# Optimization experiments

Measured on AMD Instinct MI355X. Metric: run time of the kernel, lower is better.

## Reference

```python
import jax, jax.numpy as jnp
import numpy as np

E, C, F, K = 8, 768, 3072, 2  # NUM_EXPERTS, EMBED_DIM, FFN_DIM, TOP_K


def setup_inputs() -> dict:
    key = jax.random.key(0)
    k0, k1, k2, k3 = jax.random.split(key, 4)
    B, T = 8, 2048
    return {
        "x": jax.random.normal(k0, (B, T, C), jnp.float32),
        "router_w": jax.random.normal(k1, (E, C), jnp.float32) * 0.02,
        "w1": jax.random.normal(k2, (E, C, F), jnp.float32) * 0.02,
        "b1": jnp.zeros((E, F), jnp.float32),
        "w2": jax.random.normal(k3, (E, F, C), jnp.float32) * 0.02,
        "b2": jnp.zeros((E, C), jnp.float32),
    }


def reference(x, router_w, w1, b1, w2, b2):
    # Dropout is inference-mode identity (eval). GELU is torch's exact (erf) variant.
    B, T, Cc = x.shape
    flat = x.reshape(-1, Cc)                                   # [N, C]
    logits = flat @ router_w.T                                 # [N, E]
    probs = jax.nn.softmax(logits.astype(jnp.float32), axis=-1)
    top_w, top_i = jax.lax.top_k(probs, K)                     # [N, K]
    top_w = (top_w / top_w.sum(-1, keepdims=True)).astype(x.dtype)
    out = jnp.zeros_like(flat)
    for e in range(E):
        # per-token combine weight for expert e (0 if token not routed to e)
        w_e = jnp.sum(top_w * (top_i == e), axis=-1)[:, None]  # [N, 1]
        h = jax.nn.gelu(flat @ w1[e] + b1[e], approximate=False)  # [N, F]
        out = out + w_e * (h @ w2[e] + b2[e])
    return out.reshape(B, T, Cc)
```

## Files before the change

### kernel.cpp

```cpp
#include <hip/hip_runtime.h>
#include <hip/hip_bf16.h>

#define NTOK 16384
#define CDIM 768
#define FDIM 3072
#define NEXP 8
#define NSLOT 32768
#define HBLK 128
#define MAXT256 135

typedef __attribute__((ext_vector_type(8))) short bf16x8;
typedef __attribute__((ext_vector_type(4))) float f32x4;
typedef __attribute__((ext_vector_type(8))) unsigned short u16x8;

__device__ __forceinline__ unsigned short f2bf(float f) {
  unsigned int u = __float_as_uint(f);
  u += 0x7FFFu + ((u >> 16) & 1u);
  return (unsigned short)(u >> 16);
}
__device__ __forceinline__ float bf2f(unsigned short h) {
  return __uint_as_float((unsigned int)h << 16);
}

__device__ __forceinline__ float fast_gelu(float x) {
  float x2 = x * x;
  float z = x * __builtin_fmaf(0.070565402f, x2, 1.5975981f);
  float s = __builtin_amdgcn_rcpf(1.0f + __expf(-z));
  return x * s;
}

__device__ __forceinline__ void async16(const void* g, void* l) {
  __builtin_amdgcn_global_load_lds(
      (const __attribute__((address_space(1))) unsigned int*)g,
      (__attribute__((address_space(3))) unsigned int*)l, 16, 0, 0);
}

#define BARRIER() asm volatile("s_barrier" ::: "memory")
#define VMC(n)    asm volatile("s_waitcnt vmcnt(" #n ")" ::: "memory")

__global__ __launch_bounds__(256)
void k_transpose(const float* __restrict__ src, unsigned short* __restrict__ dst,
                 int R, int Cc)
{
  __shared__ float tle[32][33];
  int e = blockIdx.z;
  int c0 = blockIdx.x * 32, r0 = blockIdx.y * 32;
  int tx = threadIdx.x & 31, ty = threadIdx.x >> 5;
  const float* s = src + (size_t)e * R * Cc;
  unsigned short* d = dst + (size_t)e * R * Cc;
#pragma unroll
  for (int i = 0; i < 4; ++i)
    tle[ty + i * 8][tx] = s[(size_t)(r0 + ty + i * 8) * Cc + c0 + tx];
  __syncthreads();
#pragma unroll
  for (int i = 0; i < 4; ++i)
    d[(size_t)(c0 + ty + i * 8) * R + r0 + tx] = f2bf(tle[tx][ty + i * 8]);
}

__global__ __launch_bounds__(256)
void k_router(const float* __restrict__ x, const float* __restrict__ rw,
              int* __restrict__ tk_e, float* __restrict__ tk_w)
{
  __shared__ float srw[NEXP * CDIM];
  int tid = threadIdx.x;
#pragma unroll
  for (int i = 0; i < (NEXP * CDIM / 4) / 256; ++i)
    ((float4*)srw)[tid + i * 256] = ((const float4*)rw)[tid + i * 256];
  __syncthreads();
  int lane = tid & 63, wid = tid >> 6;
  int t = blockIdx.x * 4 + wid;
  float a[NEXP];
#pragma unroll
  for (int e = 0; e < NEXP; ++e) a[e] = 0.f;
  const float* xr = x + (size_t)t * CDIM;
#pragma unroll
  for (int c = 0; c < CDIM / 64; ++c) {
    float xv = xr[c * 64 + lane];
#pragma unroll
    for (int e = 0; e < NEXP; ++e) a[e] += xv * srw[e * CDIM + c * 64 + lane];
  }
#pragma unroll
  for (int e = 0; e < NEXP; ++e) {
#pragma unroll
    for (int off = 32; off; off >>= 1) a[e] += __shfl_xor(a[e], off);
  }
  if (lane == 0) {
    int i0 = 0; float l0 = a[0];
#pragma unroll
    for (int e = 1; e < NEXP; ++e) if (a[e] > l0) { l0 = a[e]; i0 = e; }
    int i1 = -1; float l1 = -1e30f;
#pragma unroll
    for (int e = 0; e < NEXP; ++e) if (e != i0 && a[e] > l1) { l1 = a[e]; i1 = e; }
    float w0 = 1.f / (1.f + expf(l1 - l0));
    tk_e[2 * t] = i0;     tk_e[2 * t + 1] = i1;
    tk_w[2 * t] = w0;     tk_w[2 * t + 1] = 1.f - w0;
  }
}

__global__ __launch_bounds__(256)
void k_hist(const int* __restrict__ tk_e, int* __restrict__ blockhist)
{
  __shared__ int h[NEXP];
  int tid = threadIdx.x;
  if (tid < NEXP) h[tid] = 0;
  __syncthreads();
  int e = tk_e[blockIdx.x * 256 + tid];
  atomicAdd(&h[e], 1);
  __syncthreads();
  if (tid < NEXP) blockhist[blockIdx.x * NEXP + tid] = h[tid];
}

__global__ __launch_bounds__(512)
void k_scan2(const int* __restrict__ blockhist, int* __restrict__ counts,
             int* __restrict__ offsets, int* __restrict__ tp,
             int* __restrict__ blockbase)
{
  __shared__ int ltot[NEXP];
  __shared__ int loff[NEXP + 1];
  int tid = threadIdx.x;
  int lane = tid & 63, e = tid >> 6;
  int o0 = blockhist[lane * NEXP + e];
  int o1 = blockhist[(64 + lane) * NEXP + e];
  int h0 = o0, h1 = o1;
#pragma unroll
  for (int d = 1; d < 64; d <<= 1) { int v = __shfl_up(h0, d); if (lane >= d) h0 += v; }
  int s0 = __shfl(h0, 63);
#pragma unroll
  for (int d = 1; d < 64; d <<= 1) { int v = __shfl_up(h1, d); if (lane >= d) h1 += v; }
  h1 += s0;
  if (lane == 63) ltot[e] = h1;
  __syncthreads();
  if (tid == 0) {
    loff[0] = 0;
    int tpv = 0; tp[0] = 0;
    for (int k = 0; k < NEXP; ++k) {
      loff[k + 1] = loff[k] + ltot[k];
      counts[k] = ltot[k];
      offsets[k] = loff[k];
      tpv += (ltot[k] + 255) / 256;
      tp[k + 1] = tpv;
    }
    offsets[NEXP] = loff[NEXP];
  }
  __syncthreads();
  int base = loff[e];
  blockbase[lane * NEXP + e]        = base + h0 - o0;
  blockbase[(64 + lane) * NEXP + e] = base + h1 - o1;
}

__global__ __launch_bounds__(256)
void k_assign(const int* __restrict__ tk_e, const float* __restrict__ tk_w,
              const int* __restrict__ blockbase,
              int* __restrict__ tok2slot, float* __restrict__ slot_w,
              int* __restrict__ slot_pick)
{
  __shared__ int eh[256];
  int b = blockIdx.x, tid = threadIdx.x;
  int pick = b * 256 + tid;
  int e = tk_e[pick];
  eh[tid] = e;
  __syncthreads();
  int rank = 0;
  for (int j = 0; j < tid; ++j) rank += (eh[j] == e);
  int slot = blockbase[b * NEXP + e] + rank;
  tok2slot[pick] = slot;
  slot_w[slot] = tk_w[pick];
  slot_pick[slot] = pick;
}

__global__ __launch_bounds__(256)
void k_gather(const float* __restrict__ x, const int* __restrict__ slot_pick,
              unsigned short* __restrict__ Xg)
{
  int lane = threadIdx.x & 63, w = threadIdx.x >> 6;
#pragma unroll
  for (int i = 0; i < 8; ++i) {
    int s = blockIdx.x * 32 + i * 4 + w;
    int token = slot_pick[s] >> 1;
    const float4* src = (const float4*)(x + (size_t)token * CDIM);
    ushort4* dst = (ushort4*)(Xg + (size_t)s * CDIM);
#pragma unroll
    for (int j = 0; j < 3; ++j) {
      float4 v = src[j * 64 + lane];
      ushort4 hh;
      hh.x = f2bf(v.x); hh.y = f2bf(v.y); hh.z = f2bf(v.z); hh.w = f2bf(v.w);
      dst[j * 64 + lane] = hh;
    }
  }
}

__global__ __launch_bounds__(512, 2)
void k_gemm1(const unsigned short* __restrict__ A, int lda,
             const unsigned short* __restrict__ B, int ldb, long sB,
             const int* __restrict__ counts,
             const int* __restrict__ offsets, const int* __restrict__ tp,
             int t0, const float* __restrict__ bias, int biasStride,
             unsigned short* __restrict__ Hout, int ldh, int gx, int nwg)
{
  constexpr int KI = CDIM / 128;
  __shared__ __align__(16) char lds[131072];

  int orig = blockIdx.y * gx + blockIdx.x;
  int q = nwg >> 3, r = nwg & 7;
  int xcd = orig & 7, jj = orig >> 3;
  int wgid = (xcd < r ? xcd * (q + 1) : r * (q + 1) + (xcd - r) * q) + jj;
  const int RG = 16;
  int yT = nwg / gx;
  int gsize = gx * RG;
  int rg = wgid / gsize;
  int rem = wgid - rg * gsize;
  int rgs = yT - rg * RG; if (rgs > RG) rgs = RG;
  int bx = rem / rgs;
  int byl = rg * RG + (rem - bx * rgs);
  int by = t0 + byl;

  if (by >= tp[NEXP]) return;
  int e = 0;
  while (by >= tp[e + 1]) ++e;
  int rowbase = offsets[e];
  int m0 = (by - tp[e]) * 256;
  int n0 = bx * 256;

  const unsigned short* Bexp = B + (long)e * sB + (long)n0 * ldb;
  const unsigned short* Aexp = A + (long)(rowbase + m0) * lda;

  int tid = threadIdx.x;
  int lane = tid & 63, wid = tid >> 6;
  int wm = wid >> 2, wn = wid & 3;
  int ar = lane & 15, kg = lane >> 4;
  int arl = ar & 7;

  const char* pA[2][2];
  const char* pB[2][2];
#pragma unroll
  for (int d = 0; d < 2; ++d)
#pragma unroll
    for (int s = 0; s < 2; ++s) {
      int sw = (((s * 4 + kg) ^ arl) << 4);
      pA[d][s] = lds + d * 65536 + (wm * 128 + ar) * 128 + sw;
      pB[d][s] = lds + d * 65536 + 32768 + (wn * 64 + ar) * 128 + sw;
    }

  int srow = tid >> 3, schunk = tid & 7;
  int sswz = ((schunk ^ (srow & 7)) << 3);
  const unsigned short* srcA = Aexp + (long)srow * lda + sswz;
  const unsigned short* srcB = Bexp + (long)srow * ldb + sswz;

  auto STG_A = [&](int d, int kt, int g) {
    async16(srcA + (long)g * 64 * lda + kt * 64,
            lds + d * 65536 + g * 8192 + wid * 1024);
  };
  auto STG_B = [&](int d, int kt, int g) {
    async16(srcB + (long)g * 64 * ldb + kt * 64,
            lds + d * 65536 + 32768 + g * 8192 + wid * 1024);
  };

  f32x4 acc[8][4] = {};
  bf16x8 a[2][4], b[2][4];

#define LDA_(d, h)                                                   \
  _Pragma("unroll") for (int s = 0; s < 2; ++s)                      \
  _Pragma("unroll") for (int m = 0; m < 4; ++m)                      \
    a[s][m] = *(const bf16x8*)(pA[d][s] + (h) * 8192 + m * 2048);
#define LDB_(d, np)                                                  \
  _Pragma("unroll") for (int s = 0; s < 2; ++s)                      \
  _Pragma("unroll") for (int j = 0; j < 2; ++j)                      \
    b[s][(np) * 2 + j] = *(const bf16x8*)(pB[d][s] + ((np) * 2 + j) * 2048);
#define MM_(h, np)                                                   \
  _Pragma("unroll") for (int m = 0; m < 4; ++m)                      \
  _Pragma("unroll") for (int j = 0; j < 2; ++j) {                    \
    acc[(h)*4+m][(np)*2+j] = __builtin_amdgcn_mfma_f32_16x16x32_bf16(\
        a[0][m], b[0][(np)*2+j], acc[(h)*4+m][(np)*2+j], 0, 0, 0);   \
    acc[(h)*4+m][(np)*2+j] = __builtin_amdgcn_mfma_f32_16x16x32_bf16(\
        a[1][m], b[1][(np)*2+j], acc[(h)*4+m][(np)*2+j], 0, 0, 0); }
#define PHTAIL()  __builtin_amdgcn_s_setprio(1)
#define PHEND()   __builtin_amdgcn_s_setprio(0); BARRIER()

  STG_A(0, 0, 0); STG_A(0, 0, 1); STG_A(0, 0, 2); STG_A(0, 0, 3);
  STG_B(0, 0, 0); STG_B(0, 0, 1); STG_B(0, 0, 2); STG_B(0, 0, 3);
  STG_A(1, 1, 0); STG_A(1, 1, 1);
  VMC(2);
  BARRIER();

#pragma unroll
  for (int i = 0; i < KI; ++i) {
    const int kt1 = 2 * i + 1, kt2 = 2 * i + 2, kt3 = 2 * i + 3;
    const bool cond = (i + 1 < KI);
    LDA_(0, 0); LDB_(0, 0);
    STG_A(1, kt1, 2); STG_A(1, kt1, 3);
    BARRIER(); PHTAIL(); MM_(0, 0); PHEND();
    LDB_(0, 1);
    STG_B(1, kt1, 0); STG_B(1, kt1, 1);
    BARRIER(); PHTAIL(); MM_(0, 1); PHEND();
    LDA_(0, 1);
    STG_B(1, kt1, 2); STG_B(1, kt1, 3);
    BARRIER(); PHTAIL(); MM_(1, 0); PHEND();
    if (cond) {
      STG_A(0, kt2, 0); STG_A(0, kt2, 1);
      VMC(2);
    } else {
      VMC(0);
    }
    BARRIER(); PHTAIL(); MM_(1, 1); PHEND();
    LDA_(1, 0); LDB_(1, 0);
    if (cond) { STG_A(0, kt2, 2); STG_A(0, kt2, 3); }
    BARRIER(); PHTAIL(); MM_(0, 0); PHEND();
    LDB_(1, 1);
    if (cond) { STG_B(0, kt2, 0); STG_B(0, kt2, 1); }
    BARRIER(); PHTAIL(); MM_(0, 1); PHEND();
    LDA_(1, 1);
    if (cond) { STG_B(0, kt2, 2); STG_B(0, kt2, 3); }
    BARRIER(); PHTAIL(); MM_(1, 0); PHEND();
    if (cond) {
      STG_A(1, kt3, 0); STG_A(1, kt3, 1);
      VMC(2);
    }
    BARRIER(); PHTAIL(); MM_(1, 1); PHEND();
  }

  unsigned short* st = (unsigned short*)lds;
  __syncthreads();
#pragma unroll
  for (int pass = 0; pass < 2; ++pass) {
    if (wm == pass) {
#pragma unroll
      for (int n = 0; n < 4; ++n) {
        int col = wn * 64 + n * 16 + ar;
        float bv = bias[e * biasStride + n0 + col];
#pragma unroll
        for (int m = 0; m < 8; ++m) {
#pragma unroll
          for (int rr = 0; rr < 4; ++rr) {
            int row = m * 16 + kg * 4 + rr;
            float v = fast_gelu(acc[m][n][rr] + bv);
            st[row * 264 + col] = f2bf(v);
          }
        }
      }
    }
    __syncthreads();
    int row = tid >> 2, qq = tid & 3;
    unsigned short* drow =
        Hout + (long)(byl * 256 + pass * 128 + row) * ldh + n0 + qq * 64;
    const unsigned short* srow2 = st + row * 264 + qq * 64;
#pragma unroll
    for (int i = 0; i < 8; ++i)
      *(u16x8*)(drow + i * 8) = *(const u16x8*)(srow2 + i * 8);
    __syncthreads();
  }
#undef LDA_
#undef LDB_
#undef MM_
#undef PHTAIL
#undef PHEND
}

__global__ __launch_bounds__(512, 2)
void k_gemm2_8ph(const unsigned short* __restrict__ A, int lda,
                 const unsigned short* __restrict__ B, int ldb, long sB,
                 const int* __restrict__ counts,
                 const int* __restrict__ offsets, const int* __restrict__ tp,
                 int t0, const float* __restrict__ bias, int biasStride,
                 unsigned short* __restrict__ Yout,
                 const float* __restrict__ slot_w, int gx, int nwg)
{
  constexpr int KI = FDIM / 128;
  __shared__ __align__(16) char lds[131072];

  int orig = blockIdx.y * gx + blockIdx.x;
  int q = nwg >> 3, r = nwg & 7;
  int xcd = orig & 7, jj = orig >> 3;
  int wgid = (xcd < r ? xcd * (q + 1) : r * (q + 1) + (xcd - r) * q) + jj;
  const int RG = 16;
  int yT = nwg / gx;
  int gsize = gx * RG;
  int rg = wgid / gsize;
  int rem = wgid - rg * gsize;
  int rgs = yT - rg * RG; if (rgs > RG) rgs = RG;
  int bx = rem / rgs;
  int byl = rg * RG + (rem - bx * rgs);
  int by = t0 + byl;

  if (by >= tp[NEXP]) return;
  int e = 0;
  while (by >= tp[e + 1]) ++e;
  int cnt = counts[e];
  int rowbase = offsets[e];
  int m0 = (by - tp[e]) * 256;
  int n0 = bx * 256;

  const unsigned short* Bexp = B + (long)e * sB + (long)n0 * ldb;
  const unsigned short* Aexp = A + (long)(byl * 256) * lda;

  int tid = threadIdx.x;
  int lane = tid & 63, wid = tid >> 6;
  int wm = wid >> 2, wn = wid & 3;
  int ar = lane & 15, kg = lane >> 4;
  int arl = ar & 7;

  const char* pA[2][2];
  const char* pB[2][2];
#pragma unroll
  for (int d = 0; d < 2; ++d)
#pragma unroll
    for (int s = 0; s < 2; ++s) {
      int sw = (((s * 4 + kg) ^ arl) << 4);
      pA[d][s] = lds + d * 65536 + (wm * 128 + ar) * 128 + sw;
      pB[d][s] = lds + d * 65536 + 32768 + (wn * 64 + ar) * 128 + sw;
    }

  int srow = tid >> 3, schunk = tid & 7;
  int sswz = ((schunk ^ (srow & 7)) << 3);
  const unsigned short* srcA = Aexp + (long)srow * lda + sswz;
  const unsigned short* srcB = Bexp + (long)srow * ldb + sswz;

  auto STG_A = [&](int d, int kt, int g) {
    async16(srcA + (long)g * 64 * lda + kt * 64,
            lds + d * 65536 + g * 8192 + wid * 1024);
  };
  auto STG_B = [&](int d, int kt, int g) {
    async16(srcB + (long)g * 64 * ldb + kt * 64,
            lds + d * 65536 + 32768 + g * 8192 + wid * 1024);
  };

  f32x4 acc[8][4] = {};
  bf16x8 a[2][4], b[2][4];

#define LDA_(d, h)                                                   \
  _Pragma("unroll") for (int s = 0; s < 2; ++s)                      \
  _Pragma("unroll") for (int m = 0; m < 4; ++m)                      \
    a[s][m] = *(const bf16x8*)(pA[d][s] + (h) * 8192 + m * 2048);
#define LDB_(d, np)                                                  \
  _Pragma("unroll") for (int s = 0; s < 2; ++s)                      \
  _Pragma("unroll") for (int j = 0; j < 2; ++j)                      \
    b[s][(np) * 2 + j] = *(const bf16x8*)(pB[d][s] + ((np) * 2 + j) * 2048);
#define MM_(h, np)                                                   \
  _Pragma("unroll") for (int m = 0; m < 4; ++m)                      \
  _Pragma("unroll") for (int j = 0; j < 2; ++j) {                    \
    acc[(h)*4+m][(np)*2+j] = __builtin_amdgcn_mfma_f32_16x16x32_bf16(\
        a[0][m], b[0][(np)*2+j], acc[(h)*4+m][(np)*2+j], 0, 0, 0);   \
    acc[(h)*4+m][(np)*2+j] = __builtin_amdgcn_mfma_f32_16x16x32_bf16(\
        a[1][m], b[1][(np)*2+j], acc[(h)*4+m][(np)*2+j], 0, 0, 0); }
#define PHTAIL()  __builtin_amdgcn_s_setprio(1)
#define PHEND()   __builtin_amdgcn_s_setprio(0); BARRIER()

  STG_A(0, 0, 0); STG_A(0, 0, 1); STG_A(0, 0, 2); STG_A(0, 0, 3);
  STG_B(0, 0, 0); STG_B(0, 0, 1); STG_B(0, 0, 2); STG_B(0, 0, 3);
  STG_A(1, 1, 0); STG_A(1, 1, 1);
  VMC(2);
  BARRIER();

#pragma unroll 1
  for (int i = 0; i < KI; ++i) {
    const int kt1 = 2 * i + 1, kt2 = 2 * i + 2, kt3 = 2 * i + 3;
    const bool cond = (i + 1 < KI);
    LDA_(0, 0); LDB_(0, 0);
    STG_A(1, kt1, 2); STG_A(1, kt1, 3);
    BARRIER(); PHTAIL(); MM_(0, 0); PHEND();
    LDB_(0, 1);
    STG_B(1, kt1, 0); STG_B(1, kt1, 1);
    BARRIER(); PHTAIL(); MM_(0, 1); PHEND();
    LDA_(0, 1);
    STG_B(1, kt1, 2); STG_B(1, kt1, 3);
    BARRIER(); PHTAIL(); MM_(1, 0); PHEND();
    if (cond) {
      STG_A(0, kt2, 0); STG_A(0, kt2, 1);
      VMC(2);
    } else {
      VMC(0);
    }
    BARRIER(); PHTAIL(); MM_(1, 1); PHEND();
    LDA_(1, 0); LDB_(1, 0);
    if (cond) { STG_A(0, kt2, 2); STG_A(0, kt2, 3); }
    BARRIER(); PHTAIL(); MM_(0, 0); PHEND();
    LDB_(1, 1);
    if (cond) { STG_B(0, kt2, 0); STG_B(0, kt2, 1); }
    BARRIER(); PHTAIL(); MM_(0, 1); PHEND();
    LDA_(1, 1);
    if (cond) { STG_B(0, kt2, 2); STG_B(0, kt2, 3); }
    BARRIER(); PHTAIL(); MM_(1, 0); PHEND();
    if (cond) {
      STG_A(1, kt3, 0); STG_A(1, kt3, 1);
      VMC(2);
    }
    BARRIER(); PHTAIL(); MM_(1, 1); PHEND();
  }

  unsigned short* st = (unsigned short*)lds;
  __syncthreads();
#pragma unroll
  for (int pass = 0; pass < 2; ++pass) {
    if (wm == pass) {
#pragma unroll
      for (int m = 0; m < 8; ++m) {
#pragma unroll
        for (int rr = 0; rr < 4; ++rr) {
          int row = m * 16 + kg * 4 + rr;
          int grow = m0 + pass * 128 + row;
          float wt = (grow < cnt) ? slot_w[rowbase + grow] : 0.f;
#pragma unroll
          for (int n = 0; n < 4; ++n) {
            int col = wn * 64 + n * 16 + ar;
            float v = (acc[m][n][rr] + bias[e * biasStride + n0 + col]) * wt;
            st[row * 264 + col] = f2bf(v);
          }
        }
      }
    }
    __syncthreads();
    int row = tid >> 2, qq = tid & 3;
    int grow = m0 + pass * 128 + row;
    if (grow < cnt) {
      unsigned short* drow =
          Yout + (long)(rowbase + grow) * CDIM + n0 + qq * 64;
      const unsigned short* srow2 = st + row * 264 + qq * 64;
#pragma unroll
      for (int i = 0; i < 8; ++i)
        *(u16x8*)(drow + i * 8) = *(const u16x8*)(srow2 + i * 8);
    }
    __syncthreads();
  }
#undef LDA_
#undef LDB_
#undef MM_
#undef PHTAIL
#undef PHEND
}

__global__ __launch_bounds__(256, 3)
void k_gemm2(const unsigned short* __restrict__ A, int lda,
             const unsigned short* __restrict__ B, int ldb, long sB,
             int Ksteps, const int* __restrict__ counts,
             const int* __restrict__ offsets, const int* __restrict__ tp,
             int t0, const float* __restrict__ bias, int biasStride,
             unsigned short* __restrict__ Yout, const float* __restrict__ slot_w,
             int gx, int nwg)
{
  __shared__ __align__(16) char lds[3 * 16384];

  int orig = blockIdx.y * gx + blockIdx.x;
  int q = nwg >> 3, r = nwg & 7;
  int xcd = orig & 7, jj = orig >> 3;
  int wgid = (xcd < r ? xcd * (q + 1) : r * (q + 1) + (xcd - r) * q) + jj;
  const int RG = 16;
  int yT = nwg / gx;
  int gsize = gx * RG;
  int rg = wgid / gsize;
  int rem = wgid - rg * gsize;
  int rgs = yT - rg * RG; if (rgs > RG) rgs = RG;
  int bx = rem / rgs;
  int byl = rg * RG + (rem - bx * rgs);

  int t256l = byl >> 1, half = byl & 1;
  int by = t0 + t256l;
  if (by >= tp[NEXP]) return;
  int e = 0;
  while (by >= tp[e + 1]) ++e;
  int cnt = counts[e];
  int rowbase = offsets[e];
  int m0 = (by - tp[e]) * 256 + half * 128;
  if (m0 >= cnt) return;
  int n0 = bx * 128;

  const unsigned short* Bexp = B + (long)e * sB + (long)n0 * ldb;
  const unsigned short* Aexp = A + (long)(t256l * 256 + half * 128) * lda;

  int tid = threadIdx.x;
  int lane = tid & 63, wid = tid >> 6;
  int wm = wid >> 1, wn = wid & 1;
  int ar = lane & 15, kg = lane >> 4;
  int kgs = (kg ^ ((ar >> 1) & 3)) << 4;

  int rA0 = tid >> 2;
  int cA0 = tid & 3;
  int ksw = (cA0 ^ ((rA0 >> 1) & 3)) << 3;
  const unsigned short* As0 = Aexp + (long)rA0 * lda + ksw;
  const unsigned short* As1 = Aexp + (long)(rA0 + 64) * lda + ksw;
  const unsigned short* Bs0 = Bexp + (long)rA0 * ldb + ksw;
  const unsigned short* Bs1 = Bexp + (long)(rA0 + 64) * ldb + ksw;

  f32x4 acc[4][4] = {};

  auto STAGE = [&](int buf, int t) {
    char* bb = lds + buf * 16384;
    int ko = t * 32;
    async16(As0 + ko, bb + wid * 1024);
    async16(As1 + ko, bb + 4096 + wid * 1024);
    async16(Bs0 + ko, bb + 8192 + wid * 1024);
    async16(Bs1 + ko, bb + 12288 + wid * 1024);
  };

  STAGE(0, 0); STAGE(1, 1);
  int cur = 0, nxt2 = 2;

  for (int ks = 0; ks < Ksteps; ++ks) {
    if (ks + 1 < Ksteps) {
      asm volatile("s_waitcnt vmcnt(4)" ::: "memory");
    } else {
      asm volatile("s_waitcnt vmcnt(0)" ::: "memory");
    }
    __builtin_amdgcn_s_barrier();
    asm volatile("" ::: "memory");

    const char* bb = lds + cur * 16384;
    const char* bA = bb + (wm * 64 + ar) * 64 + kgs;
    const char* bB = bb + 8192 + (wn * 64 + ar) * 64 + kgs;
    bf16x8 af[4], bfr[4];
#pragma unroll
    for (int i = 0; i < 4; ++i) af[i] = *(const bf16x8*)(bA + i * 1024);
#pragma unroll
    for (int i = 0; i < 4; ++i) bfr[i] = *(const bf16x8*)(bB + i * 1024);

    if (ks + 2 < Ksteps) STAGE(nxt2, ks + 2);

#pragma unroll
    for (int mi = 0; mi < 4; ++mi)
#pragma unroll
      for (int ni = 0; ni < 4; ++ni)
        acc[mi][ni] = __builtin_amdgcn_mfma_f32_16x16x32_bf16(af[mi], bfr[ni],
                                                              acc[mi][ni], 0, 0, 0);
    cur = (cur == 2) ? 0 : cur + 1;
    nxt2 = (nxt2 == 2) ? 0 : nxt2 + 1;
  }

  unsigned short* st = (unsigned short*)lds;
  __syncthreads();

#pragma unroll
  for (int mi = 0; mi < 4; ++mi) {
#pragma unroll
    for (int rr = 0; rr < 4; ++rr) {
      int rowl = wm * 64 + mi * 16 + kg * 4 + rr;
      float wt = (m0 + rowl < cnt) ? slot_w[rowbase + m0 + rowl] : 0.f;
#pragma unroll
      for (int ni = 0; ni < 4; ++ni) {
        int col = wn * 64 + ni * 16 + ar;
        float v = (acc[mi][ni][rr] + bias[e * biasStride + n0 + col]) * wt;
        st[rowl * 136 + col] = f2bf(v);
      }
    }
  }
  __syncthreads();
  int row = tid >> 1, hh = tid & 1;
  if (m0 + row < cnt) {
    unsigned short* drow = Yout + (long)(rowbase + m0 + row) * CDIM + n0 + hh * 64;
    const unsigned short* srow = st + row * 136 + hh * 64;
#pragma unroll
    for (int i = 0; i < 8; ++i)
      *(u16x8*)(drow + i * 8) = *(const u16x8*)(srow + i * 8);
  }
}

__global__ __launch_bounds__(256)
void k_combine(const unsigned short* __restrict__ Y,
               const int* __restrict__ tok2slot, float* __restrict__ out)
{
  int t = blockIdx.x * 4 + (threadIdx.x >> 6);
  int lane = threadIdx.x & 63;
  int s0 = tok2slot[2 * t], s1 = tok2slot[2 * t + 1];
  const ushort4* y0 = (const ushort4*)(Y + (size_t)s0 * CDIM);
  const ushort4* y1 = (const ushort4*)(Y + (size_t)s1 * CDIM);
  float4* o = (float4*)(out + (size_t)t * CDIM);
#pragma unroll
  for (int i = 0; i < 3; ++i) {
    ushort4 aa = y0[i * 64 + lane];
    ushort4 bb = y1[i * 64 + lane];
    float4 rr;
    rr.x = bf2f(aa.x) + bf2f(bb.x);
    rr.y = bf2f(aa.y) + bf2f(bb.y);
    rr.z = bf2f(aa.z) + bf2f(bb.z);
    rr.w = bf2f(aa.w) + bf2f(bb.w);
    o[i * 64 + lane] = rr;
  }
}

extern "C" void kernel_launch(void* const* d_in, const int* in_sizes, int n_in,
                              void* d_out, int out_size, void* d_ws, size_t ws_size,
                              hipStream_t stream) {
  const float* x        = (const float*)d_in[0];
  const float* router_w = (const float*)d_in[1];
  const float* w1       = (const float*)d_in[2];
  const float* b1       = (const float*)d_in[3];
  const float* w2       = (const float*)d_in[4];
  const float* b2       = (const float*)d_in[5];
  float* out = (float*)d_out;

  char* ws = (char*)d_ws;
  size_t off = 0;
  auto alloc = [&](size_t bytes) -> void* {
    void* p = ws + off;
    off = (off + bytes + 255) & ~(size_t)255;
    return p;
  };
  int*   counts     = (int*)alloc(NEXP * 4);
  int*   offsets    = (int*)alloc((NEXP + 1) * 4);
  int*   tp         = (int*)alloc((NEXP + 1) * 4);
  int*   tk_e       = (int*)alloc((size_t)NSLOT * 4);
  float* tk_w       = (float*)alloc((size_t)NSLOT * 4);
  int*   blockhist  = (int*)alloc((size_t)HBLK * NEXP * 4);
  int*   blockbase  = (int*)alloc((size_t)HBLK * NEXP * 4);
  int*   tok2slot   = (int*)alloc((size_t)NSLOT * 4);
  float* slot_w     = (float*)alloc((size_t)NSLOT * 4);
  int*   slot_pick  = (int*)alloc((size_t)NSLOT * 4);
  unsigned short* Yslot = (unsigned short*)alloc((size_t)NSLOT * CDIM * 2);
  unsigned short* w1t = (unsigned short*)alloc((size_t)NEXP * FDIM * CDIM * 2);
  unsigned short* w2t = (unsigned short*)alloc((size_t)NEXP * CDIM * FDIM * 2);
  unsigned short* Xg  = (unsigned short*)alloc((size_t)(NSLOT + 256) * CDIM * 2);
  int TPC = 68;
  if (off + (size_t)TPC * 256 * FDIM * 2 > ws_size) TPC = 42;
  if (off + (size_t)TPC * 256 * FDIM * 2 > ws_size) TPC = 21;
  bool big = (TPC == 68);
  unsigned short* H = (unsigned short*)alloc((size_t)TPC * 256 * FDIM * 2);

  k_transpose<<<dim3(FDIM / 32, CDIM / 32, NEXP), 256, 0, stream>>>(w1, w1t, CDIM, FDIM);
  k_transpose<<<dim3(CDIM / 32, FDIM / 32, NEXP), 256, 0, stream>>>(w2, w2t, FDIM, CDIM);
  k_router<<<NTOK / 4, 256, 0, stream>>>(x, router_w, tk_e, tk_w);
  k_hist<<<HBLK, 256, 0, stream>>>(tk_e, blockhist);
  k_scan2<<<1, 512, 0, stream>>>(blockhist, counts, offsets, tp, blockbase);
  k_assign<<<HBLK, 256, 0, stream>>>(tk_e, tk_w, blockbase,
                                     tok2slot, slot_w, slot_pick);
  k_gather<<<NSLOT / 32, 256, 0, stream>>>(x, slot_pick, Xg);

  for (int t0 = 0; t0 < MAXT256; t0 += TPC) {
    int yT = (MAXT256 - t0 < TPC) ? (MAXT256 - t0) : TPC;
    int gx1 = FDIM / 256;
    k_gemm1<<<dim3(gx1, yT), 512, 0, stream>>>(
        Xg, CDIM, w1t, CDIM, (long)FDIM * CDIM,
        counts, offsets, tp, t0, b1, FDIM, H, FDIM, gx1, gx1 * yT);
    if (big) {
      int gx2 = CDIM / 256;
      k_gemm2_8ph<<<dim3(gx2, yT), 512, 0, stream>>>(
          H, FDIM, w2t, FDIM, (long)CDIM * FDIM,
          counts, offsets, tp, t0, b2, CDIM, Yslot, slot_w, gx2, gx2 * yT);
    } else {
      int gx2 = CDIM / 128;
      k_gemm2<<<dim3(gx2, 2 * yT), 256, 0, stream>>>(
          H, FDIM, w2t, FDIM, (long)CDIM * FDIM, FDIM / 32,
          counts, offsets, tp, t0, b2, CDIM, Yslot, slot_w, gx2, gx2 * 2 * yT);
    }
  }
  k_combine<<<NTOK / 4, 256, 0, stream>>>(Yslot, tok2slot, out);
}
```

Before: 628.4 us.

## Fuse token gather into GEMM1 A-loads and enlarge H chunk to single pass

```diff
diff --git a/kernel.cpp b/kernel.cpp
--- a/kernel.cpp
+++ b/kernel.cpp
@@ -55,6 +55,18 @@
 #pragma unroll
   for (int i = 0; i < 4; ++i)
     d[(size_t)(c0 + ty + i * 8) * R + r0 + tx] = f2bf(tle[tx][ty + i * 8]);
+}
+
+__global__ __launch_bounds__(256)
+void k_xbf16(const float* __restrict__ x, unsigned short* __restrict__ Xbf)
+{
+  size_t i = (size_t)blockIdx.x * 256 + threadIdx.x;
+  const float4* s = (const float4*)x;
+  float4 v0 = s[2 * i], v1 = s[2 * i + 1];
+  u16x8 h;
+  h[0] = f2bf(v0.x); h[1] = f2bf(v0.y); h[2] = f2bf(v0.z); h[3] = f2bf(v0.w);
+  h[4] = f2bf(v1.x); h[5] = f2bf(v1.y); h[6] = f2bf(v1.z); h[7] = f2bf(v1.w);
+  ((u16x8*)Xbf)[i] = h;
 }
 
 __global__ __launch_bounds__(256)
@@ -168,29 +180,9 @@
   slot_pick[slot] = pick;
 }
 
-__global__ __launch_bounds__(256)
-void k_gather(const float* __restrict__ x, const int* __restrict__ slot_pick,
-              unsigned short* __restrict__ Xg)
-{
-  int lane = threadIdx.x & 63, w = threadIdx.x >> 6;
-#pragma unroll
-  for (int i = 0; i < 8; ++i) {
-    int s = blockIdx.x * 32 + i * 4 + w;
-    int token = slot_pick[s] >> 1;
-    const float4* src = (const float4*)(x + (size_t)token * CDIM);
-    ushort4* dst = (ushort4*)(Xg + (size_t)s * CDIM);
-#pragma unroll
-    for (int j = 0; j < 3; ++j) {
-      float4 v = src[j * 64 + lane];
-      ushort4 hh;
-      hh.x = f2bf(v.x); hh.y = f2bf(v.y); hh.z = f2bf(v.z); hh.w = f2bf(v.w);
-      dst[j * 64 + lane] = hh;
-    }
-  }
-}
-
 __global__ __launch_bounds__(512, 2)
-void k_gemm1(const unsigned short* __restrict__ A, int lda,
+void k_gemm1(const unsigned short* __restrict__ Xbf,
+             const int* __restrict__ slot_pick,
              const unsigned short* __restrict__ B, int ldb, long sB,
              const int* __restrict__ counts,
              const int* __restrict__ offsets, const int* __restrict__ tp,
@@ -222,7 +214,6 @@
   int n0 = bx * 256;
 
   const unsigned short* Bexp = B + (long)e * sB + (long)n0 * ldb;
-  const unsigned short* Aexp = A + (long)(rowbase + m0) * lda;
 
   int tid = threadIdx.x;
   int lane = tid & 63, wid = tid >> 6;
@@ -243,11 +234,18 @@
 
   int srow = tid >> 3, schunk = tid & 7;
   int sswz = ((schunk ^ (srow & 7)) << 3);
-  const unsigned short* srcA = Aexp + (long)srow * lda + sswz;
+  const unsigned short* srcAg[4];
+#pragma unroll
+  for (int g = 0; g < 4; ++g) {
+    int sidx = rowbase + m0 + srow + g * 64;
+    if (sidx > NSLOT - 1) sidx = NSLOT - 1;
+    int tok = slot_pick[sidx] >> 1;
+    srcAg[g] = Xbf + (long)tok * CDIM + sswz;
+  }
   const unsigned short* srcB = Bexp + (long)srow * ldb + sswz;
 
   auto STG_A = [&](int d, int kt, int g) {
-    async16(srcA + (long)g * 64 * lda + kt * 64,
+    async16(srcAg[g] + kt * 64,
             lds + d * 65536 + g * 8192 + wid * 1024);
   };
   auto STG_B = [&](int d, int kt, int g) {
@@ -705,11 +703,12 @@
   unsigned short* Yslot = (unsigned short*)alloc((size_t)NSLOT * CDIM * 2);
   unsigned short* w1t = (unsigned short*)alloc((size_t)NEXP * FDIM * CDIM * 2);
   unsigned short* w2t = (unsigned short*)alloc((size_t)NEXP * CDIM * FDIM * 2);
-  unsigned short* Xg  = (unsigned short*)alloc((size_t)(NSLOT + 256) * CDIM * 2);
-  int TPC = 68;
+  unsigned short* Xbf = (unsigned short*)alloc((size_t)NTOK * CDIM * 2);
+  int TPC = MAXT256;
+  if (off + (size_t)TPC * 256 * FDIM * 2 > ws_size) TPC = 68;
   if (off + (size_t)TPC * 256 * FDIM * 2 > ws_size) TPC = 42;
   if (off + (size_t)TPC * 256 * FDIM * 2 > ws_size) TPC = 21;
-  bool big = (TPC == 68);
+  bool big = (TPC >= 68);
   unsigned short* H = (unsigned short*)alloc((size_t)TPC * 256 * FDIM * 2);
 
   k_transpose<<<dim3(FDIM / 32, CDIM / 32, NEXP), 256, 0, stream>>>(w1, w1t, CDIM, FDIM);
@@ -719,13 +718,13 @@
   k_scan2<<<1, 512, 0, stream>>>(blockhist, counts, offsets, tp, blockbase);
   k_assign<<<HBLK, 256, 0, stream>>>(tk_e, tk_w, blockbase,
                                      tok2slot, slot_w, slot_pick);
-  k_gather<<<NSLOT / 32, 256, 0, stream>>>(x, slot_pick, Xg);
+  k_xbf16<<<NTOK * CDIM / 8 / 256, 256, 0, stream>>>(x, Xbf);
 
   for (int t0 = 0; t0 < MAXT256; t0 += TPC) {
     int yT = (MAXT256 - t0 < TPC) ? (MAXT256 - t0) : TPC;
     int gx1 = FDIM / 256;
     k_gemm1<<<dim3(gx1, yT), 512, 0, stream>>>(
-        Xg, CDIM, w1t, CDIM, (long)FDIM * CDIM,
+        Xbf, slot_pick, w1t, CDIM, (long)FDIM * CDIM,
         counts, offsets, tp, t0, b1, FDIM, H, FDIM, gx1, gx1 * yT);
     if (big) {
       int gx2 = CDIM / 256;
```

Measured after the change: 619.8 us. About the same (-1.4%).
